# Kernel optimization log

Measured on AMD Instinct MI355X. Metric: run time of the kernel, lower is better.

## Reference

```python
import jax, jax.numpy as jnp
import numpy as np

N_EST = 5      # n_estimators
DEPTH = 6      # n_depth
LEAVES = 64    # 2 ** n_depth


def setup_inputs() -> dict:
    key = jax.random.key(0)
    ks = jax.random.split(key, 6)
    N, F, H, L, O = 131072, 256, 384, 64, 16
    X = jax.random.normal(ks[0], (N, F), jnp.float32)
    W1 = jax.random.normal(ks[1], (F, H), jnp.float32) / np.float32(np.sqrt(F))
    b1 = jnp.zeros((H,), jnp.float32)
    W2 = jax.random.normal(ks[2], (H, L), jnp.float32) / np.float32(np.sqrt(H))
    b2 = jnp.zeros((L,), jnp.float32)
    # phi[i] = random choice of n_leaves indices from arange(n_latent) without replacement
    phi = jnp.stack([jax.random.permutation(jax.random.fold_in(ks[3], i), L)[:LEAVES]
                     for i in range(N_EST)]).astype(jnp.int32)  # [E, 64]
    # pi: per-estimator leaf->label distributions (rows on the simplex, as after softmax updates)
    pi = jax.nn.softmax(jax.random.normal(ks[4], (N_EST, LEAVES, O), jnp.float32), axis=-1)
    return {"X": X, "W1": W1, "b1": b1, "W2": W2, "b2": b2, "phi": phi, "pi": pi}


def reference(X, W1, b1, W2, b2, phi, pi):
    # Backbone MLP: sigmoid -> sigmoid, as in keras.Sequential([Dense(h,'sigmoid'), Dense(l,'sigmoid')])
    h = jax.nn.sigmoid(X @ W1 + b1)          # [N, H]
    latent = jax.nn.sigmoid(h @ W2 + b2)     # [N, L]

    N = X.shape[0]
    E = phi.shape[0]
    d = latent[:, phi]                        # gather per estimator -> [N, E, 64]
    decisions = jnp.stack([d, 1.0 - d], axis=-1)  # [N, E, 64, 2] (go-left / go-right probs)

    # Soft tree routing: product of decision probs along each root->leaf path.
    # Level `lev` uses node indices [begin:begin+2**lev); index 0 is unused (matches TF code).
    mu = jnp.ones((N, E, 1, 1), X.dtype)
    begin = 1
    for lev in range(DEPTH):
        end = begin + 2 ** lev
        # reshape [N,E,k,2] -> [N,E,2k,1]; broadcast against [N,E,k_level,2] replaces tile(1,1,2)
        mu = mu.reshape(N, E, -1, 1) * decisions[:, :, begin:end, :]
        begin = end
    mu = mu.reshape(N, E, LEAVES)             # [N, E, 64] leaf arrival probabilities

    # predict: mean over estimators of mu_e @ pi_e
    return jnp.einsum('nel,elo->no', mu, pi) / E
```

## Files before the change

### kernel.cpp

```cpp
#include <hip/hip_runtime.h>
#include <hip/hip_bf16.h>
#include <stdint.h>

#define F_DIM 256
#define H_DIM 384
#define L_DIM 64
#define O_DIM 16
#define E_NUM 5
#define BM 32

#define XK_STRIDE 264
#define H_STRIDE 392
#define LAT_STRIDE 33
#define MU_STRIDE 328

typedef short bf16x8 __attribute__((ext_vector_type(8)));
typedef float f32x4 __attribute__((ext_vector_type(4)));

__device__ __forceinline__ unsigned short f2bf(float f) {
    union { float f; unsigned int u; } v; v.f = f;
    unsigned int u = v.u;
    return (unsigned short)((u + 0x7FFFu + ((u >> 16) & 1u)) >> 16);
}

__device__ __forceinline__ unsigned int pk2(float a, float b) {
#if defined(__has_builtin)
#if __has_builtin(__builtin_amdgcn_cvt_pk_bf16_f32)
    typedef __bf16 bf2 __attribute__((ext_vector_type(2)));
    bf2 p = __builtin_amdgcn_cvt_pk_bf16_f32(a, b);
    union { bf2 v; unsigned int u; } c; c.v = p;
    return c.u;
#else
    return (unsigned int)f2bf(a) | ((unsigned int)f2bf(b) << 16);
#endif
#else
    return (unsigned int)f2bf(a) | ((unsigned int)f2bf(b) << 16);
#endif
}

__device__ __forceinline__ uint2 cvt4(float4 v) {
    uint2 r; r.x = pk2(v.x, v.y); r.y = pk2(v.z, v.w); return r;
}

__device__ __forceinline__ float sigmoidf(float x) {
    return __builtin_amdgcn_rcpf(1.0f + __builtin_amdgcn_exp2f(-1.44269504088896f * x));
}

__global__ void prep_kernel(const float* __restrict__ W1, const float* __restrict__ W2,
                            const float* __restrict__ pi,
                            unsigned short* __restrict__ W1f,
                            unsigned short* __restrict__ W2f,
                            unsigned short* __restrict__ piTf) {
    __shared__ float tile[32][33];
    const int b = blockIdx.x;
    const int tid = threadIdx.x;
    const int tx = tid & 31, ty = tid >> 5;

    if (b < 120) {
        int ks, t0, nks;
        unsigned short* dst;
        if (b < 96) {
            const int fb = b / 12, hb = b % 12;
            #pragma unroll
            for (int s = 0; s < 32; s += 8)
                tile[ty + s][tx] = W1[(size_t)(fb * 32 + ty + s) * H_DIM + hb * 32 + tx];
            ks = fb; t0 = hb * 2; nks = 8; dst = W1f;
        } else {
            const int bb = b - 96, hb = bb / 2, lb = bb % 2;
            #pragma unroll
            for (int s = 0; s < 32; s += 8)
                tile[ty + s][tx] = W2[(size_t)(hb * 32 + ty + s) * L_DIM + lb * 32 + tx];
            ks = hb; t0 = lb * 2; nks = 12; dst = W2f;
        }
        __syncthreads();
        const int t_local = tid >> 7;
        const int r = (tid * 2) & 255;
        const int lane = r >> 2;
        const int e2b = r & 3;
        const int q = lane >> 4, c = lane & 15;
        const int f0 = q * 8 + e2b * 2;
        const int hl = t_local * 16 + c;
        uint2 v;
        v.x = pk2(tile[f0 + 0][hl], tile[f0 + 1][hl]);
        v.y = pk2(tile[f0 + 2][hl], tile[f0 + 3][hl]);
        const size_t off = ((size_t)((t0 + t_local) * nks + ks) * 64 + lane) * 8 + e2b * 2;
        *(uint2*)(dst + off) = v;
    } else {
        for (int i = tid; i < O_DIM * E_NUM * L_DIM; i += 256) {
            const int j = i & 7, lane = (i >> 3) & 63, ks = i >> 9;
            const int q = lane >> 4, c = lane & 15;
            const int k = ks * 32 + q * 8 + j;
            piTf[i] = f2bf(pi[k * O_DIM + c] * 0.2f);
        }
    }
}

__global__ __launch_bounds__(256, 3) void fused_kernel(
    const float* __restrict__ X,
    const unsigned short* __restrict__ W1f,
    const float* __restrict__ b1,
    const unsigned short* __restrict__ W2f,
    const float* __restrict__ b2,
    const int* __restrict__ phi,
    const unsigned short* __restrict__ piTf,
    float* __restrict__ out) {

    __shared__ __align__(16) unsigned char smem[34816];
    unsigned short* Xs  = (unsigned short*)smem;
    unsigned short* Hs  = (unsigned short*)smem;
    float*          latT = (float*)(smem + 25088);
    int*            phis = (int*)(smem + 33536);
    unsigned short* mus = (unsigned short*)smem;

    const int tid  = threadIdx.x;
    const int wave = tid >> 6;
    const int lane = tid & 63;
    const int q    = lane >> 4;
    const int c    = lane & 15;
    const int row0 = blockIdx.x * BM;

    for (int idx = tid; idx < E_NUM * L_DIM; idx += 256) phis[idx] = phi[idx];

    #pragma unroll
    for (int h = 0; h < 2; ++h) {
        float4 t0[4];
        #pragma unroll
        for (int i = 0; i < 4; ++i)
            t0[i] = *(const float4*)(X + (size_t)(row0 + wave * 8 + h * 4 + i) * F_DIM + lane * 4);
        #pragma unroll
        for (int i = 0; i < 4; ++i)
            *(uint2*)&Xs[(wave * 8 + h * 4 + i) * XK_STRIDE + lane * 4] = cvt4(t0[i]);
    }

    bf16x8 af0[6];
    #pragma unroll
    for (int i = 0; i < 6; ++i)
        af0[i] = *(const bf16x8*)(W1f + ((size_t)(wave * 48 + i * 8 + 0) * 64 + lane) * 8);

    __syncthreads();

    f32x4 acc[6][2];
    #pragma unroll
    for (int i = 0; i < 6; ++i)
        #pragma unroll
        for (int j = 0; j < 2; ++j)
            acc[i][j] = (f32x4){0.f, 0.f, 0.f, 0.f};

    {
        bf16x8 bf0[2];
        #pragma unroll
        for (int j = 0; j < 2; ++j)
            bf0[j] = *(const bf16x8*)&Xs[(j * 16 + c) * XK_STRIDE + q * 8];
        #pragma unroll
        for (int i = 0; i < 6; ++i)
            #pragma unroll
            for (int j = 0; j < 2; ++j)
                acc[i][j] = __builtin_amdgcn_mfma_f32_16x16x32_bf16(af0[i], bf0[j], acc[i][j], 0, 0, 0);
    }
    #pragma unroll 2
    for (int ks = 1; ks < 8; ++ks) {
        bf16x8 af[6];
        #pragma unroll
        for (int i = 0; i < 6; ++i)
            af[i] = *(const bf16x8*)(W1f + ((size_t)(wave * 48 + i * 8 + ks) * 64 + lane) * 8);
        bf16x8 bf_[2];
        #pragma unroll
        for (int j = 0; j < 2; ++j)
            bf_[j] = *(const bf16x8*)&Xs[(j * 16 + c) * XK_STRIDE + ks * 32 + q * 8];
        #pragma unroll
        for (int i = 0; i < 6; ++i)
            #pragma unroll
            for (int j = 0; j < 2; ++j)
                acc[i][j] = __builtin_amdgcn_mfma_f32_16x16x32_bf16(af[i], bf_[j], acc[i][j], 0, 0, 0);
    }
    __syncthreads();

    const int nbase = wave * 96;
    #pragma unroll
    for (int i = 0; i < 6; ++i) {
        const int n0 = nbase + i * 16 + q * 4;
        float4 bv = *(const float4*)(b1 + n0);
        #pragma unroll
        for (int j = 0; j < 2; ++j) {
            const int m = j * 16 + c;
            uint2 h2;
            h2.x = pk2(sigmoidf(acc[i][j][0] + bv.x), sigmoidf(acc[i][j][1] + bv.y));
            h2.y = pk2(sigmoidf(acc[i][j][2] + bv.z), sigmoidf(acc[i][j][3] + bv.w));
            *(uint2*)&Hs[m * H_STRIDE + n0] = h2;
        }
    }
    __syncthreads();

    {
        bf16x8 wfrag[12];
        #pragma unroll
        for (int ks = 0; ks < 12; ++ks)
            wfrag[ks] = *(const bf16x8*)(W2f + ((size_t)(wave * 12 + ks) * 64 + lane) * 8);
        f32x4 acc2[2];
        acc2[0] = (f32x4){0.f, 0.f, 0.f, 0.f};
        acc2[1] = (f32x4){0.f, 0.f, 0.f, 0.f};
        #pragma unroll
        for (int ks = 0; ks < 12; ++ks) {
            #pragma unroll
            for (int j = 0; j < 2; ++j) {
                bf16x8 bf_ = *(const bf16x8*)&Hs[(j * 16 + c) * H_STRIDE + ks * 32 + q * 8];
                acc2[j] = __builtin_amdgcn_mfma_f32_16x16x32_bf16(wfrag[ks], bf_, acc2[j], 0, 0, 0);
            }
        }
        const int lb = wave * 16;
        const float4 b2v = *(const float4*)(b2 + lb + q * 4);
        #pragma unroll
        for (int j = 0; j < 2; ++j) {
            const int m = j * 16 + c;
            #pragma unroll
            for (int rg = 0; rg < 4; ++rg) {
                const int l = lb + q * 4 + rg;
                latT[l * LAT_STRIDE + m] = sigmoidf(acc2[j][rg] + ((const float*)&b2v)[rg]);
            }
        }
    }
    __syncthreads();

    {
        const int r = lane & 31;
        const int e = wave * 2 + (lane >> 5);
        if (e < E_NUM) {
            float mu[64];
            mu[0] = 1.0f;
            #pragma unroll
            for (int lev = 0; lev < 6; ++lev) {
                const int w = 1 << lev;
                #pragma unroll
                for (int i = w - 1; i >= 0; --i) {
                    float d = latT[phis[e * 64 + w + i] * LAT_STRIDE + r];
                    float m = mu[i];
                    mu[2 * i + 1] = m - m * d;
                    mu[2 * i]     = m * d;
                }
            }
            #pragma unroll
            for (int j8 = 0; j8 < 8; ++j8) {
                bf16x8 v;
                #pragma unroll
                for (int t = 0; t < 4; ++t) {
                    unsigned int p = pk2(mu[j8 * 8 + 2 * t], mu[j8 * 8 + 2 * t + 1]);
                    v[2 * t]     = (short)(p & 0xFFFF);
                    v[2 * t + 1] = (short)(p >> 16);
                }
                *((bf16x8*)&mus[r * MU_STRIDE + e * 64 + j8 * 8]) = v;
            }
        }
    }
    __syncthreads();

    if (wave < 2) {
        const int mt = wave;
        bf16x8 pfrag[10];
        #pragma unroll
        for (int ks = 0; ks < 10; ++ks)
            pfrag[ks] = *(const bf16x8*)(piTf + ((size_t)ks * 64 + lane) * 8);
        f32x4 acc3 = (f32x4){0.f, 0.f, 0.f, 0.f};
        #pragma unroll
        for (int ks = 0; ks < 10; ++ks) {
            bf16x8 af = *((const bf16x8*)&mus[(mt * 16 + c) * MU_STRIDE + ks * 32 + q * 8]);
            acc3 = __builtin_amdgcn_mfma_f32_16x16x32_bf16(af, pfrag[ks], acc3, 0, 0, 0);
        }
        #pragma unroll
        for (int rg = 0; rg < 4; ++rg) {
            const int m = mt * 16 + q * 4 + rg;
            out[(size_t)(row0 + m) * O_DIM + c] = acc3[rg];
        }
    }
}

extern "C" void kernel_launch(void* const* d_in, const int* in_sizes, int n_in,
                              void* d_out, int out_size, void* d_ws, size_t ws_size,
                              hipStream_t stream) {
    (void)in_sizes; (void)n_in; (void)out_size; (void)ws_size;
    const float* X  = (const float*)d_in[0];
    const float* W1 = (const float*)d_in[1];
    const float* b1 = (const float*)d_in[2];
    const float* W2 = (const float*)d_in[3];
    const float* b2 = (const float*)d_in[4];
    const int*   phi = (const int*)d_in[5];
    const float* pi  = (const float*)d_in[6];
    float* out = (float*)d_out;

    unsigned short* W1f  = (unsigned short*)d_ws;
    unsigned short* W2f  = (unsigned short*)((char*)d_ws + 196608);
    unsigned short* piTf = (unsigned short*)((char*)d_ws + 196608 + 49152);

    prep_kernel<<<121, 256, 0, stream>>>(W1, W2, pi, W1f, W2f, piTf);

    const int nblocks = 131072 / BM;
    fused_kernel<<<nblocks, 256, 0, stream>>>(X, W1f, b1, W2f, b2, phi, piTf, out);
}
```

Before: 248.7 us.

## Double row tile to 64 with 512-thread blocks and remap wave work

Raises the rows per block from 32 to 64 and the threads per block from 256 to 512. The eight waves each compute 48 hidden columns over 64 rows, so every W1 fragment loaded from global memory feeds four MFMA column tiles instead of two. The second layer now splits work across waves by latent tile and row half, and W2 fragments are prefetched before the sigmoid store. The aim is to halve the global weight traffic per row and to add more in-flight waves, at the cost of about twice the shared memory per block, which may reduce how many blocks fit on a CU.

Result: faster. 240.7 us (-3.2%).

```diff
diff --git a/kernel.cpp b/kernel.cpp
--- a/kernel.cpp
+++ b/kernel.cpp
@@ -7,12 +7,16 @@
 #define L_DIM 64
 #define O_DIM 16
 #define E_NUM 5
-#define BM 32
+#define BM 64
 
 #define XK_STRIDE 264
 #define H_STRIDE 392
-#define LAT_STRIDE 33
+#define LAT_STRIDE 65
 #define MU_STRIDE 328
+
+#define LATT_OFF 50176
+#define PHIS_OFF 66816
+#define SMEM_BYTES 68096
 
 typedef short bf16x8 __attribute__((ext_vector_type(8)));
 typedef float f32x4 __attribute__((ext_vector_type(4)));
@@ -95,7 +99,7 @@
     }
 }
 
-__global__ __launch_bounds__(256, 3) void fused_kernel(
+__global__ __launch_bounds__(512, 4) void fused_kernel(
     const float* __restrict__ X,
     const unsigned short* __restrict__ W1f,
     const float* __restrict__ b1,
@@ -105,12 +109,12 @@
     const unsigned short* __restrict__ piTf,
     float* __restrict__ out) {
 
-    __shared__ __align__(16) unsigned char smem[34816];
+    __shared__ __align__(16) unsigned char smem[SMEM_BYTES];
     unsigned short* Xs  = (unsigned short*)smem;
     unsigned short* Hs  = (unsigned short*)smem;
-    float*          latT = (float*)(smem + 25088);
-    int*            phis = (int*)(smem + 33536);
     unsigned short* mus = (unsigned short*)smem;
+    float*          latT = (float*)(smem + LATT_OFF);
+    int*            phis = (int*)(smem + PHIS_OFF);
 
     const int tid  = threadIdx.x;
     const int wave = tid >> 6;
@@ -119,69 +123,73 @@
     const int c    = lane & 15;
     const int row0 = blockIdx.x * BM;
 
-    for (int idx = tid; idx < E_NUM * L_DIM; idx += 256) phis[idx] = phi[idx];
-
-    #pragma unroll
-    for (int h = 0; h < 2; ++h) {
-        float4 t0[4];
-        #pragma unroll
-        for (int i = 0; i < 4; ++i)
-            t0[i] = *(const float4*)(X + (size_t)(row0 + wave * 8 + h * 4 + i) * F_DIM + lane * 4);
-        #pragma unroll
-        for (int i = 0; i < 4; ++i)
-            *(uint2*)&Xs[(wave * 8 + h * 4 + i) * XK_STRIDE + lane * 4] = cvt4(t0[i]);
-    }
-
-    bf16x8 af0[6];
-    #pragma unroll
-    for (int i = 0; i < 6; ++i)
-        af0[i] = *(const bf16x8*)(W1f + ((size_t)(wave * 48 + i * 8 + 0) * 64 + lane) * 8);
-
-    __syncthreads();
-
-    f32x4 acc[6][2];
-    #pragma unroll
-    for (int i = 0; i < 6; ++i)
-        #pragma unroll
-        for (int j = 0; j < 2; ++j)
+    if (tid < E_NUM * L_DIM) phis[tid] = phi[tid];
+
+    {
+        float4 t0[8];
+        #pragma unroll
+        for (int i = 0; i < 8; ++i)
+            t0[i] = *(const float4*)(X + (size_t)(row0 + wave * 8 + i) * F_DIM + lane * 4);
+        #pragma unroll
+        for (int i = 0; i < 8; ++i)
+            *(uint2*)&Xs[(wave * 8 + i) * XK_STRIDE + lane * 4] = cvt4(t0[i]);
+    }
+
+    bf16x8 af0[3];
+    #pragma unroll
+    for (int i = 0; i < 3; ++i)
+        af0[i] = *(const bf16x8*)(W1f + ((size_t)((wave * 3 + i) * 8 + 0) * 64 + lane) * 8);
+
+    __syncthreads();
+
+    f32x4 acc[3][4];
+    #pragma unroll
+    for (int i = 0; i < 3; ++i)
+        #pragma unroll
+        for (int j = 0; j < 4; ++j)
             acc[i][j] = (f32x4){0.f, 0.f, 0.f, 0.f};
 
     {
-        bf16x8 bf0[2];
-        #pragma unroll
-        for (int j = 0; j < 2; ++j)
+        bf16x8 bf0[4];
+        #pragma unroll
+        for (int j = 0; j < 4; ++j)
             bf0[j] = *(const bf16x8*)&Xs[(j * 16 + c) * XK_STRIDE + q * 8];
         #pragma unroll
-        for (int i = 0; i < 6; ++i)
-            #pragma unroll
-            for (int j = 0; j < 2; ++j)
+        for (int i = 0; i < 3; ++i)
+            #pragma unroll
+            for (int j = 0; j < 4; ++j)
                 acc[i][j] = __builtin_amdgcn_mfma_f32_16x16x32_bf16(af0[i], bf0[j], acc[i][j], 0, 0, 0);
     }
     #pragma unroll 2
     for (int ks = 1; ks < 8; ++ks) {
-        bf16x8 af[6];
-        #pragma unroll
-        for (int i = 0; i < 6; ++i)
-            af[i] = *(const bf16x8*)(W1f + ((size_t)(wave * 48 + i * 8 + ks) * 64 + lane) * 8);
-        bf16x8 bf_[2];
-        #pragma unroll
-        for (int j = 0; j < 2; ++j)
+        bf16x8 af[3];
+        #pragma unroll
+        for (int i = 0; i < 3; ++i)
+            af[i] = *(const bf16x8*)(W1f + ((size_t)((wave * 3 + i) * 8 + ks) * 64 + lane) * 8);
+        bf16x8 bf_[4];
+        #pragma unroll
+        for (int j = 0; j < 4; ++j)
             bf_[j] = *(const bf16x8*)&Xs[(j * 16 + c) * XK_STRIDE + ks * 32 + q * 8];
         #pragma unroll
-        for (int i = 0; i < 6; ++i)
-            #pragma unroll
-            for (int j = 0; j < 2; ++j)
+        for (int i = 0; i < 3; ++i)
+            #pragma unroll
+            for (int j = 0; j < 4; ++j)
                 acc[i][j] = __builtin_amdgcn_mfma_f32_16x16x32_bf16(af[i], bf_[j], acc[i][j], 0, 0, 0);
     }
     __syncthreads();
 
-    const int nbase = wave * 96;
-    #pragma unroll
-    for (int i = 0; i < 6; ++i) {
-        const int n0 = nbase + i * 16 + q * 4;
+    const int lt = wave >> 1;
+    bf16x8 wfrag[12];
+    #pragma unroll
+    for (int ks = 0; ks < 12; ++ks)
+        wfrag[ks] = *(const bf16x8*)(W2f + ((size_t)(lt * 12 + ks) * 64 + lane) * 8);
+
+    #pragma unroll
+    for (int i = 0; i < 3; ++i) {
+        const int n0 = wave * 48 + i * 16 + q * 4;
         float4 bv = *(const float4*)(b1 + n0);
         #pragma unroll
-        for (int j = 0; j < 2; ++j) {
+        for (int j = 0; j < 4; ++j) {
             const int m = j * 16 + c;
             uint2 h2;
             h2.x = pk2(sigmoidf(acc[i][j][0] + bv.x), sigmoidf(acc[i][j][1] + bv.y));
@@ -192,10 +200,7 @@
     __syncthreads();
 
     {
-        bf16x8 wfrag[12];
-        #pragma unroll
-        for (int ks = 0; ks < 12; ++ks)
-            wfrag[ks] = *(const bf16x8*)(W2f + ((size_t)(wave * 12 + ks) * 64 + lane) * 8);
+        const int mbase = (wave & 1) * 2;
         f32x4 acc2[2];
         acc2[0] = (f32x4){0.f, 0.f, 0.f, 0.f};
         acc2[1] = (f32x4){0.f, 0.f, 0.f, 0.f};
@@ -203,57 +208,54 @@
         for (int ks = 0; ks < 12; ++ks) {
             #pragma unroll
             for (int j = 0; j < 2; ++j) {
-                bf16x8 bf_ = *(const bf16x8*)&Hs[(j * 16 + c) * H_STRIDE + ks * 32 + q * 8];
+                bf16x8 bf_ = *(const bf16x8*)&Hs[((mbase + j) * 16 + c) * H_STRIDE + ks * 32 + q * 8];
                 acc2[j] = __builtin_amdgcn_mfma_f32_16x16x32_bf16(wfrag[ks], bf_, acc2[j], 0, 0, 0);
             }
         }
-        const int lb = wave * 16;
-        const float4 b2v = *(const float4*)(b2 + lb + q * 4);
+        const float4 b2v = *(const float4*)(b2 + lt * 16 + q * 4);
         #pragma unroll
         for (int j = 0; j < 2; ++j) {
-            const int m = j * 16 + c;
+            const int m = (mbase + j) * 16 + c;
             #pragma unroll
             for (int rg = 0; rg < 4; ++rg) {
-                const int l = lb + q * 4 + rg;
+                const int l = lt * 16 + q * 4 + rg;
                 latT[l * LAT_STRIDE + m] = sigmoidf(acc2[j][rg] + ((const float*)&b2v)[rg]);
             }
         }
     }
     __syncthreads();
 
-    {
-        const int r = lane & 31;
-        const int e = wave * 2 + (lane >> 5);
-        if (e < E_NUM) {
-            float mu[64];
-            mu[0] = 1.0f;
-            #pragma unroll
-            for (int lev = 0; lev < 6; ++lev) {
-                const int w = 1 << lev;
-                #pragma unroll
-                for (int i = w - 1; i >= 0; --i) {
-                    float d = latT[phis[e * 64 + w + i] * LAT_STRIDE + r];
-                    float m = mu[i];
-                    mu[2 * i + 1] = m - m * d;
-                    mu[2 * i]     = m * d;
-                }
-            }
-            #pragma unroll
-            for (int j8 = 0; j8 < 8; ++j8) {
-                bf16x8 v;
-                #pragma unroll
-                for (int t = 0; t < 4; ++t) {
-                    unsigned int p = pk2(mu[j8 * 8 + 2 * t], mu[j8 * 8 + 2 * t + 1]);
-                    v[2 * t]     = (short)(p & 0xFFFF);
-                    v[2 * t + 1] = (short)(p >> 16);
-                }
-                *((bf16x8*)&mus[r * MU_STRIDE + e * 64 + j8 * 8]) = v;
-            }
-        }
-    }
-    __syncthreads();
-
-    if (wave < 2) {
+    if (wave < E_NUM) {
+        const int e = wave;
+        const int r = lane;
+        float mu[64];
+        mu[0] = 1.0f;
+        #pragma unroll
+        for (int lev = 0; lev < 6; ++lev) {
+            const int w = 1 << lev;
+            #pragma unroll
+            for (int i = w - 1; i >= 0; --i) {
+                float d = latT[phis[e * 64 + w + i] * LAT_STRIDE + r];
+                float m = mu[i];
+                mu[2 * i + 1] = m - m * d;
+                mu[2 * i]     = m * d;
+            }
+        }
+        #pragma unroll
+        for (int j8 = 0; j8 < 8; ++j8) {
+            bf16x8 v;
+            #pragma unroll
+            for (int t = 0; t < 4; ++t) {
+                unsigned int p = pk2(mu[j8 * 8 + 2 * t], mu[j8 * 8 + 2 * t + 1]);
+                v[2 * t]     = (short)(p & 0xFFFF);
+                v[2 * t + 1] = (short)(p >> 16);
+            }
+            *((bf16x8*)&mus[r * MU_STRIDE + e * 64 + j8 * 8]) = v;
+        }
+    }
+    __syncthreads();
+
+    if (wave < 4) {
         const int mt = wave;
         bf16x8 pfrag[10];
         #pragma unroll
@@ -293,5 +295,5 @@
     prep_kernel<<<121, 256, 0, stream>>>(W1, W2, pi, W1f, W2f, piTf);
 
     const int nblocks = 131072 / BM;
-    fused_kernel<<<nblocks, 256, 0, stream>>>(X, W1f, b1, W2f, b2, phi, piTf, out);
-}
+    fused_kernel<<<nblocks, 512, 0, stream>>>(X, W1f, b1, W2f, b2, phi, piTf, out);
+}
```
